# Kernel optimization log

Measured on AMD Instinct MI355X. Metric: run time of the kernel, lower is better.

Reference implementation:

```python
import jax, jax.numpy as jnp
import numpy as np

B = 8192      # batch size
D = 512       # feature dim == num_classes (centers is [C, C] in the original)
C = 512       # num_classes
MARGIN = 1.0


def setup_inputs() -> dict:
    key = jax.random.key(0)
    k1, k2, k3 = jax.random.split(key, 3)
    inputs = jax.random.normal(k1, (B, D), dtype=jnp.float32)
    targets = jax.random.randint(k2, (B,), 0, C)
    centers = jax.random.normal(k3, (C, D), dtype=jnp.float32)  # learned param
    return {"inputs": inputs, "targets": targets, "centers": centers}


def reference(inputs, targets, centers):
    # centers_batch[j] = centers[targets[j]]  (gather rows)
    cb = centers[targets]                                   # [B, D]
    # dist[i, j] = || inputs[i] - cb[j] ||_2, computed via the expanded form
    # (||a||^2 + ||b||^2 - 2 a.b) so we never materialize a [B, B, D] tensor.
    sq = ((inputs * inputs).sum(-1)[:, None]
          + (cb * cb).sum(-1)[None, :]
          - 2.0 * (inputs @ cb.T))                          # [B, B]
    dist = jnp.sqrt(jnp.clip(sq, 1e-12))                    # clamp(min=1e-12).sqrt()

    # mask[i, j] = (targets[i] == targets[j]); note original indexes dist[i][mask[i]]
    mask = targets[:, None] == targets[None, :]             # [B, B] bool
    dist_ap = jnp.max(jnp.where(mask, dist, -jnp.inf), axis=1)   # hardest positive per row
    dist_an = jnp.min(jnp.where(mask, jnp.inf, dist), axis=1)    # hardest negative per row

    # MarginRankingLoss(margin)(dist_an, dist_ap, y=1) = mean(relu(dist_ap - dist_an + margin))
    loss = jnp.mean(jnp.maximum(0.0, dist_ap - dist_an + MARGIN))
    prec = jnp.mean((dist_an > dist_ap).astype(jnp.float32))
    return loss, prec
```

## Files before the change

### kernel.cpp

```cpp
#include <hip/hip_runtime.h>
#include <hip/hip_bf16.h>

#define NB 8192
#define ND 512
#define NC 512
#define NCT 8
#define MARGIN_F 1.0f
#define BIGF 3.0e38f

typedef __attribute__((ext_vector_type(8))) short bf16x8;
typedef __attribute__((ext_vector_type(4))) float f32x4;

__device__ __forceinline__ unsigned fkey(float f) {
    unsigned u = __float_as_uint(f);
    unsigned mask = (u & 0x80000000u) ? 0xFFFFFFFFu : 0x80000000u;
    return u ^ mask;
}
__device__ __forceinline__ float finv(unsigned k) {
    unsigned mask = (k & 0x80000000u) ? 0x80000000u : 0xFFFFFFFFu;
    return __uint_as_float(k ^ mask);
}
__device__ __forceinline__ unsigned short f2bf(float f) {
    __hip_bfloat16 h = __float2bfloat16(f);
    return __builtin_bit_cast(unsigned short, h);
}

#define GLOAD_LDS16(g, l)                                                    \
    __builtin_amdgcn_global_load_lds(                                        \
        (const __attribute__((address_space(1))) void*)(g),                  \
        (__attribute__((address_space(3))) void*)(l), 16, 0, 0)

__global__ __launch_bounds__(256) void k0_prep(
    const float* __restrict__ inputs, const int* __restrict__ targets,
    const float* __restrict__ centers,
    unsigned short* __restrict__ inB, unsigned short* __restrict__ cenB,
    float* __restrict__ rsq, float* __restrict__ csq,
    unsigned* __restrict__ counts)
{
    const int bid = blockIdx.x;
    const int tid = threadIdx.x;

    if (bid == 2176) {
        __shared__ unsigned hist[NC];
        for (int i = tid; i < NC; i += 256) hist[i] = 0u;
        __syncthreads();
        for (int i = tid; i < NB; i += 256) atomicAdd(&hist[targets[i]], 1u);
        __syncthreads();
        for (int i = tid; i < NC; i += 256) counts[i] = hist[i];
        return;
    }

    const int wave = tid >> 6, lane = tid & 63;
    const float* src;
    unsigned short* dst;
    float* sqdst;
    int row;
    bool is_input = (bid < 2048);
    if (is_input) {
        row   = bid * 4 + wave;
        src   = inputs + (size_t)row * ND;
        dst   = inB + (size_t)row * ND;
        sqdst = rsq + row;
    } else {
        row   = (bid - 2048) * 4 + wave;
        src   = centers + (size_t)row * ND;
        dst   = cenB + (size_t)row * ND;
        sqdst = csq + row;
    }

    float4 v1 = ((const float4*)src)[lane];
    float4 v2 = ((const float4*)src)[lane + 64];
    float s = v1.x*v1.x + v1.y*v1.y + v1.z*v1.z + v1.w*v1.w
            + v2.x*v2.x + v2.y*v2.y + v2.z*v2.z + v2.w*v2.w;

    ushort4 o1, o2;
    o1.x = f2bf(v1.x); o1.y = f2bf(v1.y); o1.z = f2bf(v1.z); o1.w = f2bf(v1.w);
    o2.x = f2bf(v2.x); o2.y = f2bf(v2.y); o2.z = f2bf(v2.z); o2.w = f2bf(v2.w);
    ((ushort4*)dst)[lane]      = o1;
    ((ushort4*)dst)[lane + 64] = o2;

    #pragma unroll
    for (int off = 32; off > 0; off >>= 1) s += __shfl_down(s, off);
    if (lane == 0) *sqdst = s;
}

__global__ __launch_bounds__(256) void k2_mfma(
    const unsigned short* __restrict__ Ain, const unsigned short* __restrict__ cenB,
    const int* __restrict__ targets, const unsigned* __restrict__ counts,
    const float* __restrict__ csq,
    float* __restrict__ partmin, float* __restrict__ apval)
{
    __shared__ __align__(16) unsigned short As[128 * 32];
    __shared__ __align__(16) unsigned short Bs[64 * 32];
    __shared__ int      tgtL[128];
    __shared__ float    csqL[64];
    __shared__ unsigned ldsmin[128];

    const int tid  = threadIdx.x;
    const int w    = tid >> 6;
    const int lane = tid & 63;
    const int wm   = w >> 1;
    const int wn   = w & 1;
    const int qd   = lane >> 4;
    const int ln   = lane & 15;

    const int bid   = blockIdx.x;
    const int rbase = (bid & 63) * 128;
    const int ct    = bid >> 6;
    const int cbase = ct * 64;

    if (tid < 128) { tgtL[tid] = targets[rbase + tid]; ldsmin[tid] = 0xFFFFFFFFu; }
    if (tid < 64) {
        const int c = cbase + tid;
        csqL[tid] = (counts[c] > 0u) ? csq[c] : BIGF;
    }

    const int arow0 = w * 32 + (lane >> 2);
    const int brow  = w * 16 + (lane >> 2);
    const int scol  = (lane & 3) * 8;
    const unsigned short* gA0 = Ain  + (size_t)(rbase + arow0)      * ND + scol;
    const unsigned short* gA1 = Ain  + (size_t)(rbase + arow0 + 16) * ND + scol;
    const unsigned short* gB  = cenB + (size_t)(cbase + brow)       * ND + scol;
    unsigned short* lA0 = &As[(w * 32)      * 32];
    unsigned short* lA1 = &As[(w * 32 + 16) * 32];
    unsigned short* lB  = &Bs[(w * 16)      * 32];

    f32x4 acc[4][2] = {};

    for (int kb = 0; kb < ND; kb += 32) {
        __syncthreads();
        GLOAD_LDS16(gA0 + kb, lA0);
        GLOAD_LDS16(gA1 + kb, lA1);
        GLOAD_LDS16(gB  + kb, lB);
        __syncthreads();

        bf16x8 a[4], b[2];
        #pragma unroll
        for (int i = 0; i < 4; ++i)
            a[i] = *(const bf16x8*)&As[(wm * 64 + i * 16 + ln) * 32 + qd * 8];
        #pragma unroll
        for (int j = 0; j < 2; ++j)
            b[j] = *(const bf16x8*)&Bs[(wn * 32 + j * 16 + ln) * 32 + qd * 8];
        #pragma unroll
        for (int i = 0; i < 4; ++i)
            #pragma unroll
            for (int j = 0; j < 2; ++j)
                acc[i][j] = __builtin_amdgcn_mfma_f32_16x16x32_bf16(a[i], b[j], acc[i][j], 0, 0, 0);
    }

    #pragma unroll
    for (int i = 0; i < 4; ++i) {
        #pragma unroll
        for (int r = 0; r < 4; ++r) {
            const int rlocal = wm * 64 + i * 16 + qd * 4 + r;
            const int grow   = rbase + rlocal;
            const int tr     = tgtL[rlocal];
            float m = BIGF;
            #pragma unroll
            for (int j = 0; j < 2; ++j) {
                const int clocal = wn * 32 + j * 16 + ln;
                const float val = csqL[clocal] - 2.0f * acc[i][j][r];
                if (cbase + clocal == tr) {
                    apval[grow] = val;
                } else {
                    m = fminf(m, val);
                }
            }
            #pragma unroll
            for (int off = 1; off < 16; off <<= 1)
                m = fminf(m, __shfl_xor(m, off));
            if (ln == 0) atomicMin(&ldsmin[rlocal], fkey(m));
        }
    }
    __syncthreads();
    if (tid < 128)
        partmin[(size_t)(rbase + tid) * NCT + ct] = finv(ldsmin[tid]);
}

__global__ __launch_bounds__(1024) void k3_final(
    const float* __restrict__ rsq, const float* __restrict__ partmin,
    const float* __restrict__ apval, float* __restrict__ out)
{
    __shared__ float sl[1024];
    __shared__ float sp[1024];
    const int tid = threadIdx.x;
    float a = 0.0f, p = 0.0f;
    #pragma unroll
    for (int it = 0; it < NB / 1024; ++it) {
        const int r = it * 1024 + tid;
        const float4* pm = (const float4*)&partmin[(size_t)r * NCT];
        float4 m0 = pm[0], m1 = pm[1];
        float m = fminf(fminf(fminf(m0.x, m0.y), fminf(m0.z, m0.w)),
                        fminf(fminf(m1.x, m1.y), fminf(m1.z, m1.w)));
        float s  = rsq[r];
        float an = sqrtf(fmaxf(s + m,        1e-12f));
        float ap = sqrtf(fmaxf(s + apval[r], 1e-12f));
        a += fmaxf(0.0f, ap - an + MARGIN_F);
        p += (an > ap) ? 1.0f : 0.0f;
    }
    sl[tid] = a; sp[tid] = p;
    __syncthreads();
    #pragma unroll
    for (int s = 512; s > 0; s >>= 1) {
        if (tid < s) { sl[tid] += sl[tid + s]; sp[tid] += sp[tid + s]; }
        __syncthreads();
    }
    if (tid == 0) {
        out[0] = sl[0] / (float)NB;
        out[1] = sp[0] / (float)NB;
    }
}

extern "C" void kernel_launch(void* const* d_in, const int* in_sizes, int n_in,
                              void* d_out, int out_size, void* d_ws, size_t ws_size,
                              hipStream_t stream) {
    const float* inputs  = (const float*)d_in[0];
    const int*   targets = (const int*)d_in[1];
    const float* centers = (const float*)d_in[2];
    float* out = (float*)d_out;

    char* wp = (char*)d_ws;
    unsigned short* inB     = (unsigned short*)(wp);
    unsigned short* cenB    = (unsigned short*)(wp + 8388608);
    float*          rsq     = (float*)(wp + 8912896);
    float*          csqv    = (float*)(wp + 8945664);
    unsigned*       counts  = (unsigned*)(wp + 8947712);
    float*          apval   = (float*)(wp + 8949760);
    float*          partmin = (float*)(wp + 8982528);

    k0_prep<<<2177, 256, 0, stream>>>(inputs, targets, centers,
                                      inB, cenB, rsq, csqv, counts);
    k2_mfma<<<512, 256, 0, stream>>>(inB, cenB, targets, counts, csqv,
                                     partmin, apval);
    k3_final<<<1, 1024, 0, stream>>>(rsq, partmin, apval, out);
}
```

Measured before the change: 93.15 us.

## Double-buffer GEMM LDS tiles and parallelize final reduction across blocks

The MFMA kernel now uses two LDS buffers, issuing the global-to-LDS loads for the next K slice before computing on the current one, so it needs one barrier per iteration instead of two. The final reduction kernel moves from a single 1024-thread block to 32 blocks. These use wave shuffles and fixed-point 64-bit atomics, with a last-block counter writing the result. Accumulators are zeroed in the prep kernel. The costs are more LDS per block, reliance on the global_load_lds completing before the barrier, and fixed-point quantisation of the loss sum.

```diff
diff --git a/kernel.cpp b/kernel.cpp
--- a/kernel.cpp
+++ b/kernel.cpp
@@ -7,6 +7,7 @@
 #define NCT 8
 #define MARGIN_F 1.0f
 #define BIGF 3.0e38f
+#define K3_BLOCKS 32
 
 typedef __attribute__((ext_vector_type(8))) short bf16x8;
 typedef __attribute__((ext_vector_type(4))) float f32x4;
@@ -35,13 +36,14 @@
     const float* __restrict__ centers,
     unsigned short* __restrict__ inB, unsigned short* __restrict__ cenB,
     float* __restrict__ rsq, float* __restrict__ csq,
-    unsigned* __restrict__ counts)
+    unsigned* __restrict__ counts, unsigned long long* __restrict__ accums)
 {
     const int bid = blockIdx.x;
     const int tid = threadIdx.x;
 
     if (bid == 2176) {
         __shared__ unsigned hist[NC];
+        if (tid < 3) accums[tid] = 0ull;
         for (int i = tid; i < NC; i += 256) hist[i] = 0u;
         __syncthreads();
         for (int i = tid; i < NB; i += 256) atomicAdd(&hist[targets[i]], 1u);
@@ -90,8 +92,8 @@
     const float* __restrict__ csq,
     float* __restrict__ partmin, float* __restrict__ apval)
 {
-    __shared__ __align__(16) unsigned short As[128 * 32];
-    __shared__ __align__(16) unsigned short Bs[64 * 32];
+    __shared__ __align__(16) unsigned short As[2][128 * 32];
+    __shared__ __align__(16) unsigned short Bs[2][64 * 32];
     __shared__ int      tgtL[128];
     __shared__ float    csqL[64];
     __shared__ unsigned ldsmin[128];
@@ -121,32 +123,41 @@
     const unsigned short* gA0 = Ain  + (size_t)(rbase + arow0)      * ND + scol;
     const unsigned short* gA1 = Ain  + (size_t)(rbase + arow0 + 16) * ND + scol;
     const unsigned short* gB  = cenB + (size_t)(cbase + brow)       * ND + scol;
-    unsigned short* lA0 = &As[(w * 32)      * 32];
-    unsigned short* lA1 = &As[(w * 32 + 16) * 32];
-    unsigned short* lB  = &Bs[(w * 16)      * 32];
 
     f32x4 acc[4][2] = {};
 
-    for (int kb = 0; kb < ND; kb += 32) {
+#define STAGE(buf, kb) do {                                                  \
+        GLOAD_LDS16(gA0 + (kb), &As[buf][(w * 32)      * 32]);               \
+        GLOAD_LDS16(gA1 + (kb), &As[buf][(w * 32 + 16) * 32]);               \
+        GLOAD_LDS16(gB  + (kb), &Bs[buf][(w * 16)      * 32]);               \
+    } while (0)
+
+#define COMPUTE(buf) do {                                                    \
+        bf16x8 a[4], b[2];                                                   \
+        _Pragma("unroll")                                                    \
+        for (int i = 0; i < 4; ++i)                                          \
+            a[i] = *(const bf16x8*)&As[buf][(wm * 64 + i * 16 + ln) * 32 + qd * 8]; \
+        _Pragma("unroll")                                                    \
+        for (int j = 0; j < 2; ++j)                                          \
+            b[j] = *(const bf16x8*)&Bs[buf][(wn * 32 + j * 16 + ln) * 32 + qd * 8]; \
+        _Pragma("unroll")                                                    \
+        for (int i = 0; i < 4; ++i)                                          \
+            _Pragma("unroll")                                                \
+            for (int j = 0; j < 2; ++j)                                      \
+                acc[i][j] = __builtin_amdgcn_mfma_f32_16x16x32_bf16(a[i], b[j], acc[i][j], 0, 0, 0); \
+    } while (0)
+
+    STAGE(0, 0);
+    __syncthreads();
+    int cur = 0;
+    #pragma unroll
+    for (int kb = 32; kb < ND; kb += 32) {
+        STAGE(cur ^ 1, kb);
+        COMPUTE(cur);
         __syncthreads();
-        GLOAD_LDS16(gA0 + kb, lA0);
-        GLOAD_LDS16(gA1 + kb, lA1);
-        GLOAD_LDS16(gB  + kb, lB);
-        __syncthreads();
-
-        bf16x8 a[4], b[2];
-        #pragma unroll
-        for (int i = 0; i < 4; ++i)
-            a[i] = *(const bf16x8*)&As[(wm * 64 + i * 16 + ln) * 32 + qd * 8];
-        #pragma unroll
-        for (int j = 0; j < 2; ++j)
-            b[j] = *(const bf16x8*)&Bs[(wn * 32 + j * 16 + ln) * 32 + qd * 8];
-        #pragma unroll
-        for (int i = 0; i < 4; ++i)
-            #pragma unroll
-            for (int j = 0; j < 2; ++j)
-                acc[i][j] = __builtin_amdgcn_mfma_f32_16x16x32_bf16(a[i], b[j], acc[i][j], 0, 0, 0);
-    }
+        cur ^= 1;
+    }
+    COMPUTE(cur);
 
     #pragma unroll
     for (int i = 0; i < 4; ++i) {
@@ -177,37 +188,46 @@
         partmin[(size_t)(rbase + tid) * NCT + ct] = finv(ldsmin[tid]);
 }
 
-__global__ __launch_bounds__(1024) void k3_final(
+__global__ __launch_bounds__(256) void k3_final(
     const float* __restrict__ rsq, const float* __restrict__ partmin,
-    const float* __restrict__ apval, float* __restrict__ out)
+    const float* __restrict__ apval, unsigned long long* __restrict__ acc,
+    float* __restrict__ out)
 {
-    __shared__ float sl[1024];
-    __shared__ float sp[1024];
     const int tid = threadIdx.x;
-    float a = 0.0f, p = 0.0f;
-    #pragma unroll
-    for (int it = 0; it < NB / 1024; ++it) {
-        const int r = it * 1024 + tid;
-        const float4* pm = (const float4*)&partmin[(size_t)r * NCT];
-        float4 m0 = pm[0], m1 = pm[1];
-        float m = fminf(fminf(fminf(m0.x, m0.y), fminf(m0.z, m0.w)),
-                        fminf(fminf(m1.x, m1.y), fminf(m1.z, m1.w)));
-        float s  = rsq[r];
-        float an = sqrtf(fmaxf(s + m,        1e-12f));
-        float ap = sqrtf(fmaxf(s + apval[r], 1e-12f));
-        a += fmaxf(0.0f, ap - an + MARGIN_F);
-        p += (an > ap) ? 1.0f : 0.0f;
-    }
-    sl[tid] = a; sp[tid] = p;
+    const int r   = blockIdx.x * 256 + tid;
+
+    const float4* pm = (const float4*)&partmin[(size_t)r * NCT];
+    float4 m0 = pm[0], m1 = pm[1];
+    float m = fminf(fminf(fminf(m0.x, m0.y), fminf(m0.z, m0.w)),
+                    fminf(fminf(m1.x, m1.y), fminf(m1.z, m1.w)));
+    float s  = rsq[r];
+    float an = sqrtf(fmaxf(s + m,        1e-12f));
+    float ap = sqrtf(fmaxf(s + apval[r], 1e-12f));
+    float a = fmaxf(0.0f, ap - an + MARGIN_F);
+    float p = (an > ap) ? 1.0f : 0.0f;
+
+    #pragma unroll
+    for (int off = 32; off > 0; off >>= 1) {
+        a += __shfl_down(a, off);
+        p += __shfl_down(p, off);
+    }
+    __shared__ float sa[4], sp[4];
+    const int w = tid >> 6, lane = tid & 63;
+    if (lane == 0) { sa[w] = a; sp[w] = p; }
     __syncthreads();
-    #pragma unroll
-    for (int s = 512; s > 0; s >>= 1) {
-        if (tid < s) { sl[tid] += sl[tid + s]; sp[tid] += sp[tid + s]; }
-        __syncthreads();
-    }
     if (tid == 0) {
-        out[0] = sl[0] / (float)NB;
-        out[1] = sp[0] / (float)NB;
+        float A = sa[0] + sa[1] + sa[2] + sa[3];
+        float P = sp[0] + sp[1] + sp[2] + sp[3];
+        atomicAdd(&acc[0], (unsigned long long)((double)A * 4294967296.0 + 0.5));
+        atomicAdd(&acc[1], (unsigned long long)(P + 0.5f));
+        __threadfence();
+        unsigned* ctr = (unsigned*)&acc[2];
+        if (atomicAdd(ctr, 1u) == K3_BLOCKS - 1) {
+            unsigned long long ls = atomicAdd(&acc[0], 0ull);
+            unsigned long long ps = atomicAdd(&acc[1], 0ull);
+            out[0] = (float)((double)ls / (4294967296.0 * (double)NB));
+            out[1] = (float)((double)ps / (double)NB);
+        }
     }
 }
 
@@ -227,10 +247,11 @@
     unsigned*       counts  = (unsigned*)(wp + 8947712);
     float*          apval   = (float*)(wp + 8949760);
     float*          partmin = (float*)(wp + 8982528);
+    unsigned long long* accums = (unsigned long long*)(wp + 9244672);
 
     k0_prep<<<2177, 256, 0, stream>>>(inputs, targets, centers,
-                                      inB, cenB, rsq, csqv, counts);
+                                      inB, cenB, rsq, csqv, counts, accums);
     k2_mfma<<<512, 256, 0, stream>>>(inB, cenB, targets, counts, csqv,
                                      partmin, apval);
-    k3_final<<<1, 1024, 0, stream>>>(rsq, partmin, apval, out);
-}
+    k3_final<<<K3_BLOCKS, 256, 0, stream>>>(rsq, partmin, apval, accums, out);
+}
```

New measurement: 93.83 us. No clear change (+0.7%).

## Fuse input conversion, GEMM and final reduction into one kernel per row block

Applied to the files above, without the earlier changes.

Input rows are now converted to bf16 inside the GEMM kernel and written into swizzled LDS, so the bf16 copy of the inputs is no longer written to and read back from global memory. Each block now handles 32 rows against all 512 centers, double-buffering the center tiles in LDS. The last-block reduction uses fixed-point atomics, which removes the per-row partial-min buffer and the single-block final kernel. The cost is large LDS use per block and only 256 blocks, which lowers occupancy. Every block also re-reads all of the bf16 centers.

```diff
diff --git a/kernel.cpp b/kernel.cpp
--- a/kernel.cpp
+++ b/kernel.cpp
@@ -4,11 +4,14 @@
 #define NB 8192
 #define ND 512
 #define NC 512
-#define NCT 8
 #define MARGIN_F 1.0f
 #define BIGF 3.0e38f
+#define BM 32
+#define NBLK 256
+#define NTHR 512
 
 typedef __attribute__((ext_vector_type(8))) short bf16x8;
+typedef __attribute__((ext_vector_type(8))) unsigned short u16x8;
 typedef __attribute__((ext_vector_type(4))) float f32x4;
 
 __device__ __forceinline__ unsigned fkey(float f) {
@@ -30,18 +33,17 @@
         (const __attribute__((address_space(1))) void*)(g),                  \
         (__attribute__((address_space(3))) void*)(l), 16, 0, 0)
 
-__global__ __launch_bounds__(256) void k0_prep(
-    const float* __restrict__ inputs, const int* __restrict__ targets,
-    const float* __restrict__ centers,
-    unsigned short* __restrict__ inB, unsigned short* __restrict__ cenB,
-    float* __restrict__ rsq, float* __restrict__ csq,
-    unsigned* __restrict__ counts)
+__global__ __launch_bounds__(256) void k0c(
+    const float* __restrict__ centers, const int* __restrict__ targets,
+    unsigned short* __restrict__ cenB, float* __restrict__ csq,
+    unsigned* __restrict__ counts, unsigned long long* __restrict__ accums)
 {
     const int bid = blockIdx.x;
     const int tid = threadIdx.x;
 
-    if (bid == 2176) {
+    if (bid == 128) {
         __shared__ unsigned hist[NC];
+        if (tid < 3) accums[tid] = 0ull;
         for (int i = tid; i < NC; i += 256) hist[i] = 0u;
         __syncthreads();
         for (int i = tid; i < NB; i += 256) atomicAdd(&hist[targets[i]], 1u);
@@ -51,22 +53,9 @@
     }
 
     const int wave = tid >> 6, lane = tid & 63;
-    const float* src;
-    unsigned short* dst;
-    float* sqdst;
-    int row;
-    bool is_input = (bid < 2048);
-    if (is_input) {
-        row   = bid * 4 + wave;
-        src   = inputs + (size_t)row * ND;
-        dst   = inB + (size_t)row * ND;
-        sqdst = rsq + row;
-    } else {
-        row   = (bid - 2048) * 4 + wave;
-        src   = centers + (size_t)row * ND;
-        dst   = cenB + (size_t)row * ND;
-        sqdst = csq + row;
-    }
+    const int row = bid * 4 + wave;
+    const float* src = centers + (size_t)row * ND;
+    unsigned short* dst = cenB + (size_t)row * ND;
 
     float4 v1 = ((const float4*)src)[lane];
     float4 v2 = ((const float4*)src)[lane + 64];
@@ -81,87 +70,118 @@
 
     #pragma unroll
     for (int off = 32; off > 0; off >>= 1) s += __shfl_down(s, off);
-    if (lane == 0) *sqdst = s;
-}
-
-__global__ __launch_bounds__(256) void k2_mfma(
-    const unsigned short* __restrict__ Ain, const unsigned short* __restrict__ cenB,
-    const int* __restrict__ targets, const unsigned* __restrict__ counts,
-    const float* __restrict__ csq,
-    float* __restrict__ partmin, float* __restrict__ apval)
+    if (lane == 0) csq[row] = s;
+}
+
+__global__ __launch_bounds__(NTHR) void k2f(
+    const float* __restrict__ inputs, const int* __restrict__ targets,
+    const unsigned short* __restrict__ cenB, const unsigned* __restrict__ counts,
+    const float* __restrict__ csq, unsigned long long* __restrict__ acc3,
+    float* __restrict__ out)
 {
-    __shared__ __align__(16) unsigned short As[128 * 32];
-    __shared__ __align__(16) unsigned short Bs[64 * 32];
-    __shared__ int      tgtL[128];
-    __shared__ float    csqL[64];
-    __shared__ unsigned ldsmin[128];
+    __shared__ __align__(16) unsigned short As[BM * ND];
+    __shared__ __align__(16) unsigned short Bs[2][NC * 32];
+    __shared__ float    csqL[NC];
+    __shared__ float    rsqL[BM];
+    __shared__ float    apL[BM];
+    __shared__ int      tgtL[BM];
+    __shared__ unsigned anL[BM];
 
     const int tid  = threadIdx.x;
     const int w    = tid >> 6;
     const int lane = tid & 63;
-    const int wm   = w >> 1;
-    const int wn   = w & 1;
     const int qd   = lane >> 4;
     const int ln   = lane & 15;
-
-    const int bid   = blockIdx.x;
-    const int rbase = (bid & 63) * 128;
-    const int ct    = bid >> 6;
-    const int cbase = ct * 64;
-
-    if (tid < 128) { tgtL[tid] = targets[rbase + tid]; ldsmin[tid] = 0xFFFFFFFFu; }
-    if (tid < 64) {
-        const int c = cbase + tid;
-        csqL[tid] = (counts[c] > 0u) ? csq[c] : BIGF;
-    }
-
-    const int arow0 = w * 32 + (lane >> 2);
-    const int brow  = w * 16 + (lane >> 2);
-    const int scol  = (lane & 3) * 8;
-    const unsigned short* gA0 = Ain  + (size_t)(rbase + arow0)      * ND + scol;
-    const unsigned short* gA1 = Ain  + (size_t)(rbase + arow0 + 16) * ND + scol;
-    const unsigned short* gB  = cenB + (size_t)(cbase + brow)       * ND + scol;
-    unsigned short* lA0 = &As[(w * 32)      * 32];
-    unsigned short* lA1 = &As[(w * 32 + 16) * 32];
-    unsigned short* lB  = &Bs[(w * 16)      * 32];
-
-    f32x4 acc[4][2] = {};
-
+    const int rbase = blockIdx.x * BM;
+
+    const unsigned short* gBsrc[4];
+    #pragma unroll
+    for (int t = 0; t < 4; ++t) {
+        const int s     = w * 256 + t * 64 + lane;
+        const int rslot = s >> 2, qs = s & 3;
+        const int c     = (rslot & ~7) | (((rslot >> 1) & 3) | ((rslot & 1) << 2));
+        const int ql    = qs ^ (c & 3);
+        gBsrc[t] = cenB + (size_t)c * ND + ql * 8;
+    }
+
+#define STAGE_B(buf, kb) do {                                                \
+        _Pragma("unroll")                                                    \
+        for (int t = 0; t < 4; ++t)                                          \
+            GLOAD_LDS16(gBsrc[t] + (kb), &Bs[buf][(w * 256 + t * 64) * 8]);  \
+    } while (0)
+
+    STAGE_B(0, 0);
+
+    {
+        const int row = tid >> 4;
+        const int seg = tid & 15;
+        const float* asrc = inputs + (size_t)(rbase + row) * ND + seg * 32;
+        float ss = 0.0f;
+        #pragma unroll
+        for (int k = 0; k < 4; ++k) {
+            float4 u = ((const float4*)asrc)[k * 2];
+            float4 v = ((const float4*)asrc)[k * 2 + 1];
+            ss += u.x*u.x + u.y*u.y + u.z*u.z + u.w*u.w
+                + v.x*v.x + v.y*v.y + v.z*v.z + v.w*v.w;
+            u16x8 pk;
+            pk[0] = f2bf(u.x); pk[1] = f2bf(u.y); pk[2] = f2bf(u.z); pk[3] = f2bf(u.w);
+            pk[4] = f2bf(v.x); pk[5] = f2bf(v.y); pk[6] = f2bf(v.z); pk[7] = f2bf(v.w);
+            int byte = row * 1024 + (seg * 32 + k * 8) * 2;
+            byte ^= (row & 7) << 4;
+            *(u16x8*)((char*)As + byte) = pk;
+        }
+        ss += __shfl_down(ss, 8); ss += __shfl_down(ss, 4);
+        ss += __shfl_down(ss, 2); ss += __shfl_down(ss, 1);
+        if (seg == 0) rsqL[row] = ss;
+    }
+    csqL[tid] = (counts[tid] > 0u) ? csq[tid] : BIGF;
+    if (tid < BM) { tgtL[tid] = targets[rbase + tid]; anL[tid] = 0xFFFFFFFFu; }
+    __syncthreads();
+
+    int boff[4];
+    #pragma unroll
+    for (int j = 0; j < 4; ++j) {
+        const int c     = w * 64 + j * 16 + ln;
+        const int rslot = (c & ~7) | (((c << 1) & 6) | ((c >> 2) & 1));
+        boff[j] = rslot * 64 + ((qd ^ (c & 3)) * 16);
+    }
+
+    f32x4 acc[2][4] = {};
+    int cur = 0;
+    #pragma unroll
     for (int kb = 0; kb < ND; kb += 32) {
+        if (kb + 32 < ND) STAGE_B(cur ^ 1, kb + 32);
+        bf16x8 a[2], b[4];
+        #pragma unroll
+        for (int i = 0; i < 2; ++i) {
+            int byte = ((i * 16 + ln) * 1024 + kb * 2 + qd * 16) ^ ((ln & 7) << 4);
+            a[i] = *(const bf16x8*)((const char*)As + byte);
+        }
+        #pragma unroll
+        for (int j = 0; j < 4; ++j)
+            b[j] = *(const bf16x8*)((const char*)&Bs[cur][0] + boff[j]);
+        #pragma unroll
+        for (int i = 0; i < 2; ++i)
+            #pragma unroll
+            for (int j = 0; j < 4; ++j)
+                acc[i][j] = __builtin_amdgcn_mfma_f32_16x16x32_bf16(a[i], b[j], acc[i][j], 0, 0, 0);
         __syncthreads();
-        GLOAD_LDS16(gA0 + kb, lA0);
-        GLOAD_LDS16(gA1 + kb, lA1);
-        GLOAD_LDS16(gB  + kb, lB);
-        __syncthreads();
-
-        bf16x8 a[4], b[2];
-        #pragma unroll
-        for (int i = 0; i < 4; ++i)
-            a[i] = *(const bf16x8*)&As[(wm * 64 + i * 16 + ln) * 32 + qd * 8];
-        #pragma unroll
-        for (int j = 0; j < 2; ++j)
-            b[j] = *(const bf16x8*)&Bs[(wn * 32 + j * 16 + ln) * 32 + qd * 8];
-        #pragma unroll
-        for (int i = 0; i < 4; ++i)
-            #pragma unroll
-            for (int j = 0; j < 2; ++j)
-                acc[i][j] = __builtin_amdgcn_mfma_f32_16x16x32_bf16(a[i], b[j], acc[i][j], 0, 0, 0);
-    }
-
-    #pragma unroll
-    for (int i = 0; i < 4; ++i) {
+        cur ^= 1;
+    }
+
+    #pragma unroll
+    for (int i = 0; i < 2; ++i) {
         #pragma unroll
         for (int r = 0; r < 4; ++r) {
-            const int rlocal = wm * 64 + i * 16 + qd * 4 + r;
-            const int grow   = rbase + rlocal;
+            const int rlocal = i * 16 + qd * 4 + r;
             const int tr     = tgtL[rlocal];
             float m = BIGF;
             #pragma unroll
-            for (int j = 0; j < 2; ++j) {
-                const int clocal = wn * 32 + j * 16 + ln;
-                const float val = csqL[clocal] - 2.0f * acc[i][j][r];
-                if (cbase + clocal == tr) {
-                    apval[grow] = val;
+            for (int j = 0; j < 4; ++j) {
+                const int c = w * 64 + j * 16 + ln;
+                const float val = csqL[c] - 2.0f * acc[i][j][r];
+                if (c == tr) {
+                    apL[rlocal] = val;
                 } else {
                     m = fminf(m, val);
                 }
@@ -169,45 +189,38 @@
             #pragma unroll
             for (int off = 1; off < 16; off <<= 1)
                 m = fminf(m, __shfl_xor(m, off));
-            if (ln == 0) atomicMin(&ldsmin[rlocal], fkey(m));
+            if (ln == 0) atomicMin(&anL[rlocal], fkey(m));
         }
     }
     __syncthreads();
-    if (tid < 128)
-        partmin[(size_t)(rbase + tid) * NCT + ct] = finv(ldsmin[tid]);
-}
-
-__global__ __launch_bounds__(1024) void k3_final(
-    const float* __restrict__ rsq, const float* __restrict__ partmin,
-    const float* __restrict__ apval, float* __restrict__ out)
-{
-    __shared__ float sl[1024];
-    __shared__ float sp[1024];
-    const int tid = threadIdx.x;
-    float a = 0.0f, p = 0.0f;
-    #pragma unroll
-    for (int it = 0; it < NB / 1024; ++it) {
-        const int r = it * 1024 + tid;
-        const float4* pm = (const float4*)&partmin[(size_t)r * NCT];
-        float4 m0 = pm[0], m1 = pm[1];
-        float m = fminf(fminf(fminf(m0.x, m0.y), fminf(m0.z, m0.w)),
-                        fminf(fminf(m1.x, m1.y), fminf(m1.z, m1.w)));
-        float s  = rsq[r];
-        float an = sqrtf(fmaxf(s + m,        1e-12f));
-        float ap = sqrtf(fmaxf(s + apval[r], 1e-12f));
-        a += fmaxf(0.0f, ap - an + MARGIN_F);
-        p += (an > ap) ? 1.0f : 0.0f;
-    }
-    sl[tid] = a; sp[tid] = p;
-    __syncthreads();
-    #pragma unroll
-    for (int s = 512; s > 0; s >>= 1) {
-        if (tid < s) { sl[tid] += sl[tid + s]; sp[tid] += sp[tid + s]; }
-        __syncthreads();
-    }
-    if (tid == 0) {
-        out[0] = sl[0] / (float)NB;
-        out[1] = sp[0] / (float)NB;
+
+    if (tid < 64) {
+        double a = 0.0, p = 0.0;
+        if (tid < BM) {
+            const float mv = finv(anL[tid]);
+            const float s  = rsqL[tid];
+            const float an = sqrtf(fmaxf(s + mv,        1e-12f));
+            const float ap = sqrtf(fmaxf(s + apL[tid],  1e-12f));
+            a = (double)fmaxf(0.0f, ap - an + MARGIN_F);
+            p = (an > ap) ? 1.0 : 0.0;
+        }
+        #pragma unroll
+        for (int off = 32; off > 0; off >>= 1) {
+            a += __shfl_down(a, off);
+            p += __shfl_down(p, off);
+        }
+        if (tid == 0) {
+            atomicAdd(&acc3[0], (unsigned long long)(a * 4294967296.0 + 0.5));
+            atomicAdd(&acc3[1], (unsigned long long)(p + 0.5));
+            __threadfence();
+            unsigned* ctr = (unsigned*)&acc3[2];
+            if (atomicAdd(ctr, 1u) == NBLK - 1) {
+                unsigned long long ls = atomicAdd(&acc3[0], 0ull);
+                unsigned long long ps = atomicAdd(&acc3[1], 0ull);
+                out[0] = (float)((double)ls / (4294967296.0 * (double)NB));
+                out[1] = (float)((double)ps / (double)NB);
+            }
+        }
     }
 }
 
@@ -220,17 +233,12 @@
     float* out = (float*)d_out;
 
     char* wp = (char*)d_ws;
-    unsigned short* inB     = (unsigned short*)(wp);
-    unsigned short* cenB    = (unsigned short*)(wp + 8388608);
-    float*          rsq     = (float*)(wp + 8912896);
-    float*          csqv    = (float*)(wp + 8945664);
-    unsigned*       counts  = (unsigned*)(wp + 8947712);
-    float*          apval   = (float*)(wp + 8949760);
-    float*          partmin = (float*)(wp + 8982528);
-
-    k0_prep<<<2177, 256, 0, stream>>>(inputs, targets, centers,
-                                      inB, cenB, rsq, csqv, counts);
-    k2_mfma<<<512, 256, 0, stream>>>(inB, cenB, targets, counts, csqv,
-                                     partmin, apval);
-    k3_final<<<1, 1024, 0, stream>>>(rsq, partmin, apval, out);
-}
+    unsigned short* cenB   = (unsigned short*)(wp);
+    float*          csqv   = (float*)(wp + 524288);
+    unsigned*       counts = (unsigned*)(wp + 526336);
+    unsigned long long* accums = (unsigned long long*)(wp + 528384);
+
+    k0c<<<129, 256, 0, stream>>>(centers, targets, cenB, csqv, counts, accums);
+    k2f<<<NBLK, NTHR, 0, stream>>>(inputs, targets, cenB, counts, csqv,
+                                   accums, out);
+}
```

After: 99.76 us. 1.07x slower.
